# Kernel optimization log

Hardware: AMD Instinct MI355X
Metric: run time of the kernel (lower is better)

The kernel has to match this reference:

```python
import jax, jax.numpy as jnp
import numpy as np

H = 1024   # GRU hidden size
Z = 1024   # latent z dim
A = 4      # action dim
F = 30     # number of expert MLPs / max horizon
DIN = Z + H      # 2048, expert MLP input
DH = 512         # expert MLP hidden
EIN = H + 94     # evalMLP input (belief + pos/ori one-hot)
EH = 512
EOUT = 94


def setup_inputs() -> dict:
    key = jax.random.key(0)
    ks = jax.random.split(key, 20)
    s = 0.02
    inp = {
        "b_t": jax.random.normal(ks[0], (1, H), jnp.float32),
        "a_t": jax.random.normal(ks[1], (F, A), jnp.float32),
        "z_tp1_pos": jax.random.normal(ks[2], (F, Z), jnp.float32),
        "z_tp1_neg": jax.random.normal(ks[3], (F, Z), jnp.float32),
        "init_pos_ori": jax.random.uniform(ks[4], (1, 94), jnp.float32),
        # action GRU params (PyTorch layout: W_ih (3H, A), W_hh (3H, H))
        "gru_Wih": jax.random.normal(ks[5], (3 * H, A), jnp.float32) * s,
        "gru_Whh": jax.random.normal(ks[6], (3 * H, H), jnp.float32) * s,
        "gru_bih": jax.random.normal(ks[7], (3 * H,), jnp.float32) * s,
        "gru_bhh": jax.random.normal(ks[8], (3 * H,), jnp.float32) * s,
        # 30 stacked expert MLPs: Linear(DIN,DH)+ReLU+Linear(DH,1)
        "mlp_W1": jax.random.normal(ks[9], (F, DIN, DH), jnp.float32) * s,
        "mlp_b1": jax.random.normal(ks[10], (F, DH), jnp.float32) * s,
        "mlp_W2": jax.random.normal(ks[11], (F, DH, 1), jnp.float32) * s,
        "mlp_b2": jax.random.normal(ks[12], (F, 1), jnp.float32) * s,
        # evalMLP: Linear(EIN,EH)+ReLU+Linear(EH,EOUT)+sigmoid
        "eval_W1": jax.random.normal(ks[13], (EIN, EH), jnp.float32) * s,
        "eval_b1": jax.random.normal(ks[14], (EH,), jnp.float32) * s,
        "eval_W2": jax.random.normal(ks[15], (EH, EOUT), jnp.float32) * s,
        "eval_b2": jax.random.normal(ks[16], (EOUT,), jnp.float32) * s,
        "f": F,
    }
    return inp


def _gru(x, h0, Wih, Whh, bih, bhh):
    # x: (T, A), h0: (H,) -> outputs (T, H). PyTorch nn.GRU cell math.
    def step(h, xt):
        gi = Wih @ xt + bih          # (3H,)
        gh = Whh @ h + bhh           # (3H,)
        ir, iz, inn = jnp.split(gi, 3)
        hr, hz, hn = jnp.split(gh, 3)
        r = jax.nn.sigmoid(ir + hr)
        z = jax.nn.sigmoid(iz + hz)
        n = jnp.tanh(inn + r * hn)
        h_new = (1.0 - z) * n + z * h
        return h_new, h_new
    _, hs = jax.lax.scan(step, h0, x)
    return hs


def _experts(x, W1, b1, W2, b2, f):
    # x: (f, DIN); expert i applied to row i only (grouped batch-1 GEMMs).
    h = jax.nn.relu(jnp.einsum('fi,fih->fh', x, W1[:f]) + b1[:f])
    return jnp.einsum('fh,fho->fo', h, W2[:f]) + b2[:f]   # (f, 1) logits


def reference(b_t, a_t, z_tp1_pos, z_tp1_neg, init_pos_ori,
              gru_Wih, gru_Whh, gru_bih, gru_bhh,
              mlp_W1, mlp_b1, mlp_W2, mlp_b2,
              eval_W1, eval_b1, eval_W2, eval_b2, f):
    a_gru = _gru(a_t[:f], b_t[0], gru_Wih, gru_Whh, gru_bih, gru_bhh)  # (f, H)
    z_pos = jnp.concatenate([z_tp1_pos[:f], a_gru], axis=1)           # (f, Z+H)
    pred_positive = _experts(z_pos, mlp_W1, mlp_b1, mlp_W2, mlp_b2, f)
    z_neg = jnp.concatenate([z_tp1_neg[:f], a_gru], axis=1)
    pred_negative = _experts(z_neg, mlp_W1, mlp_b1, mlp_W2, mlp_b2, f)
    # eval branch uses b_t.detach()
    eval_in = jnp.concatenate([jax.lax.stop_gradient(b_t), init_pos_ori], axis=1)
    eh = jax.nn.relu(eval_in @ eval_W1 + eval_b1)
    pred_xytheta = jax.nn.sigmoid(eh @ eval_W2 + eval_b2)             # (1, 94)
    return pred_positive, pred_negative, pred_xytheta
```

## Files before the change

### kernel.cpp

```cpp
#include <hip/hip_runtime.h>
#include <math.h>

constexpr int kH    = 1024;
constexpr int kZ    = 1024;
constexpr int kA    = 4;
constexpr int kF    = 30;
constexpr int kDIN  = 2048;
constexpr int kDH   = 512;
constexpr int kEIN  = 1118;
constexpr int kEH   = 512;
constexpr int kEOUT = 94;

constexpr size_t GI_OFF   = 0;
constexpr size_t AGRU_OFF = GI_OFF + (size_t)kF*3*kH;
constexpr size_t HACC_OFF = AGRU_OFF + (size_t)kF*kH;
constexpr size_t EHA_OFF  = HACC_OFF + (size_t)kF*2*kDH;

__device__ __forceinline__ float sigmoidf_(float x) { return 1.0f / (1.0f + __expf(-x)); }

__device__ __forceinline__ float wave_reduce(float v) {
#pragma unroll
  for (int off = 32; off > 0; off >>= 1) v += __shfl_down(v, off, 64);
  return v;
}

__global__ __launch_bounds__(256) void gi_kernel(const float* __restrict__ Wih,
                                                 const float* __restrict__ bih,
                                                 const float* __restrict__ a_t,
                                                 float* __restrict__ gi,
                                                 const int* __restrict__ fptr) {
  int idx = blockIdx.x * 256 + threadIdx.x;
  if (idx >= kF * 3 * kH) return;
  int t = idx / (3 * kH);
  int r = idx - t * (3 * kH);
  if (t >= *fptr) return;
  float acc = bih[r];
#pragma unroll
  for (int k = 0; k < kA; k++) acc += Wih[r * kA + k] * a_t[t * kA + k];
  gi[idx] = acc;
}

__global__ __launch_bounds__(256) void gru_step(const float* __restrict__ Whh,
                                                const float* __restrict__ bhh,
                                                const float* __restrict__ gi,
                                                const float* __restrict__ b_t,
                                                float* __restrict__ agru,
                                                int t,
                                                const int* __restrict__ fptr) {
  if (t >= *fptr) return;
  const float* hprev = (t == 0) ? b_t : (agru + (size_t)(t - 1) * kH);
  int wave = threadIdx.x >> 6;
  int lane = threadIdx.x & 63;
  int j = blockIdx.x * 4 + wave;

  const float4* wr = (const float4*)(Whh + (size_t)j * kH);
  const float4* wz = (const float4*)(Whh + (size_t)(j + kH) * kH);
  const float4* wn = (const float4*)(Whh + (size_t)(j + 2 * kH) * kH);
  const float4* hv = (const float4*)hprev;

  float accr = 0.f, accz = 0.f, accn = 0.f;
#pragma unroll
  for (int k = lane; k < kH / 4; k += 64) {
    float4 hh = hv[k];
    float4 a = wr[k]; accr += a.x * hh.x + a.y * hh.y + a.z * hh.z + a.w * hh.w;
    float4 b = wz[k]; accz += b.x * hh.x + b.y * hh.y + b.z * hh.z + b.w * hh.w;
    float4 c = wn[k]; accn += c.x * hh.x + c.y * hh.y + c.z * hh.z + c.w * hh.w;
  }
  accr = wave_reduce(accr);
  accz = wave_reduce(accz);
  accn = wave_reduce(accn);

  if (lane == 0) {
    const float* git = gi + (size_t)t * 3 * kH;
    float gr = git[j] + accr + bhh[j];
    float gz = git[kH + j] + accz + bhh[kH + j];
    float hn = accn + bhh[2 * kH + j];
    float inn = git[2 * kH + j];
    float r = sigmoidf_(gr);
    float z = sigmoidf_(gz);
    float n = tanhf(inn + r * hn);
    agru[(size_t)t * kH + j] = (1.0f - z) * n + z * hprev[j];
  }
}

constexpr int EXP_SPLIT = 8;
constexpr int EVAL_SPLIT = 8;

__global__ __launch_bounds__(512) void stage1(const float* __restrict__ zpos,
                                              const float* __restrict__ zneg,
                                              const float* __restrict__ agru,
                                              const float* __restrict__ W1,
                                              const float* __restrict__ b_t,
                                              const float* __restrict__ ipo,
                                              const float* __restrict__ eW1,
                                              float* __restrict__ hacc,
                                              float* __restrict__ ehacc,
                                              const int* __restrict__ fptr) {
  int b = blockIdx.x;
  int tid = threadIdx.x;
  __shared__ float xs_p[256];
  __shared__ float xs_n[256];

  if (b < kF * EXP_SPLIT) {
    int i = b >> 3;
    int part = b & 7;
    if (i >= *fptr) return;
    int r0 = part * 256;
    if (tid < 256) {
      int r = r0 + tid;
      float xp, xn;
      if (r < kZ) { xp = zpos[(size_t)i * kZ + r]; xn = zneg[(size_t)i * kZ + r]; }
      else        { float v = agru[(size_t)i * kH + (r - kZ)]; xp = v; xn = v; }
      xs_p[tid] = xp;
      xs_n[tid] = xn;
    }
    __syncthreads();
    float ap = 0.f, an = 0.f;
    const float* w = W1 + ((size_t)i * kDIN + r0) * kDH + tid;
#pragma unroll 4
    for (int r = 0; r < 256; r++) {
      float wv = w[(size_t)r * kDH];
      ap += xs_p[r] * wv;
      an += xs_n[r] * wv;
    }
    atomicAdd(&hacc[((size_t)i * 2 + 0) * kDH + tid], ap);
    atomicAdd(&hacc[((size_t)i * 2 + 1) * kDH + tid], an);
  } else {
    int part = b - kF * EXP_SPLIT;
    int r0 = part * 140;
    int nrows = min(140, kEIN - r0);
    if (tid < nrows) {
      int r = r0 + tid;
      xs_p[tid < 256 ? tid : 0] = 0.f;
    }
    __shared__ float xs[140];
    if (tid < nrows) {
      int r = r0 + tid;
      xs[tid] = (r < kH) ? b_t[r] : ipo[r - kH];
    }
    __syncthreads();
    float acc = 0.f;
    const float* w = eW1 + (size_t)r0 * kEH + tid;
    for (int r = 0; r < nrows; r++) acc += xs[r] * w[(size_t)r * kEH];
    atomicAdd(&ehacc[tid], acc);
  }
}

__global__ __launch_bounds__(512) void stage2(const float* __restrict__ hacc,
                                              const float* __restrict__ ehacc,
                                              const float* __restrict__ b1,
                                              const float* __restrict__ W2,
                                              const float* __restrict__ b2,
                                              const float* __restrict__ eb1,
                                              const float* __restrict__ eW2,
                                              const float* __restrict__ eb2,
                                              float* __restrict__ out,
                                              const int* __restrict__ fptr) {
  int b = blockIdx.x;
  int tid = threadIdx.x;
  int f = *fptr;
  if (b < kF) {
    int i = b;
    if (i >= f) return;
    float bias = b1[(size_t)i * kDH + tid];
    float hp = fmaxf(hacc[((size_t)i * 2 + 0) * kDH + tid] + bias, 0.f);
    float hn = fmaxf(hacc[((size_t)i * 2 + 1) * kDH + tid] + bias, 0.f);
    float w = W2[(size_t)i * kDH + tid];
    float pp = hp * w, pn = hn * w;
    pp = wave_reduce(pp);
    pn = wave_reduce(pn);
    __shared__ float redp[8];
    __shared__ float redn[8];
    int wave = tid >> 6, lane = tid & 63;
    if (lane == 0) { redp[wave] = pp; redn[wave] = pn; }
    __syncthreads();
    if (tid == 0) {
      float sp = 0.f, sn = 0.f;
#pragma unroll
      for (int k = 0; k < 8; k++) { sp += redp[k]; sn += redn[k]; }
      out[i] = sp + b2[i];
      out[f + i] = sn + b2[i];
    }
  } else {
    if (tid < kEOUT) {
      float acc = eb2[tid];
      for (int h = 0; h < kEH; h++) {
        float eh = fmaxf(ehacc[h] + eb1[h], 0.f);
        acc += eh * eW2[(size_t)h * kEOUT + tid];
      }
      out[2 * f + tid] = sigmoidf_(acc);
    }
  }
}

extern "C" void kernel_launch(void* const* d_in, const int* in_sizes, int n_in,
                              void* d_out, int out_size, void* d_ws, size_t ws_size,
                              hipStream_t stream) {
  const float* b_t    = (const float*)d_in[0];
  const float* a_t    = (const float*)d_in[1];
  const float* zpos   = (const float*)d_in[2];
  const float* zneg   = (const float*)d_in[3];
  const float* ipo    = (const float*)d_in[4];
  const float* gWih   = (const float*)d_in[5];
  const float* gWhh   = (const float*)d_in[6];
  const float* gbih   = (const float*)d_in[7];
  const float* gbhh   = (const float*)d_in[8];
  const float* mW1    = (const float*)d_in[9];
  const float* mb1    = (const float*)d_in[10];
  const float* mW2    = (const float*)d_in[11];
  const float* mb2    = (const float*)d_in[12];
  const float* eW1    = (const float*)d_in[13];
  const float* eb1    = (const float*)d_in[14];
  const float* eW2    = (const float*)d_in[15];
  const float* eb2    = (const float*)d_in[16];
  const int*   fptr   = (const int*)d_in[17];

  float* ws   = (float*)d_ws;
  float* gi   = ws + GI_OFF;
  float* agru = ws + AGRU_OFF;
  float* hacc = ws + HACC_OFF;
  float* ehacc= ws + EHA_OFF;
  float* out  = (float*)d_out;

  hipMemsetAsync(hacc, 0, (size_t)(kF * 2 * kDH + kEH) * sizeof(float), stream);

  gi_kernel<<<(kF * 3 * kH + 255) / 256, 256, 0, stream>>>(gWih, gbih, a_t, gi, fptr);

  for (int t = 0; t < kF; t++) {
    gru_step<<<kH / 4, 256, 0, stream>>>(gWhh, gbhh, gi, b_t, agru, t, fptr);
  }

  stage1<<<kF * EXP_SPLIT + EVAL_SPLIT, 512, 0, stream>>>(zpos, zneg, agru, mW1, b_t,
                                                          ipo, eW1, hacc, ehacc, fptr);

  stage2<<<kF + 1, 512, 0, stream>>>(hacc, ehacc, mb1, mW2, mb2, eb1, eW2, eb2, out, fptr);
}
```

Baseline: 399.8 us.

## Replace per-step GRU launches with persistent kernel using grid barrier

The 30 separate gru_step launches and the gi_kernel are replaced by one persistent kernel of 64 blocks. Each block keeps its slice of the recurrent weights in registers, computes its input-gate projections up front into shared memory, and advances timesteps with a global atomic counter barrier. This is meant to remove per-timestep launch overhead and repeated weight reloads from memory. It depends on all 64 blocks being resident at once and adds the cost of a spin barrier on every step.

Result: slower. 445.2 us (+11.3%).

```diff
diff --git a/kernel.cpp b/kernel.cpp
--- a/kernel.cpp
+++ b/kernel.cpp
@@ -11,10 +11,14 @@
 constexpr int kEH   = 512;
 constexpr int kEOUT = 94;
 
-constexpr size_t GI_OFF   = 0;
-constexpr size_t AGRU_OFF = GI_OFF + (size_t)kF*3*kH;
-constexpr size_t HACC_OFF = AGRU_OFF + (size_t)kF*kH;
-constexpr size_t EHA_OFF  = HACC_OFF + (size_t)kF*2*kDH;
+constexpr int NB  = 64;
+constexpr int BT  = 1024;
+constexpr int JPB = 16;
+
+constexpr size_t AGRU_OFF = 0;
+constexpr size_t HACC_OFF = AGRU_OFF + (size_t)kF * kH;
+constexpr size_t EHA_OFF  = HACC_OFF + (size_t)kF * 2 * kDH;
+constexpr size_t BAR_OFF  = EHA_OFF + kEH;
 
 __device__ __forceinline__ float sigmoidf_(float x) { return 1.0f / (1.0f + __expf(-x)); }
 
@@ -24,66 +28,91 @@
   return v;
 }
 
-__global__ __launch_bounds__(256) void gi_kernel(const float* __restrict__ Wih,
-                                                 const float* __restrict__ bih,
-                                                 const float* __restrict__ a_t,
-                                                 float* __restrict__ gi,
-                                                 const int* __restrict__ fptr) {
-  int idx = blockIdx.x * 256 + threadIdx.x;
-  if (idx >= kF * 3 * kH) return;
-  int t = idx / (3 * kH);
-  int r = idx - t * (3 * kH);
-  if (t >= *fptr) return;
-  float acc = bih[r];
-#pragma unroll
-  for (int k = 0; k < kA; k++) acc += Wih[r * kA + k] * a_t[t * kA + k];
-  gi[idx] = acc;
-}
-
-__global__ __launch_bounds__(256) void gru_step(const float* __restrict__ Whh,
-                                                const float* __restrict__ bhh,
-                                                const float* __restrict__ gi,
-                                                const float* __restrict__ b_t,
-                                                float* __restrict__ agru,
-                                                int t,
-                                                const int* __restrict__ fptr) {
-  if (t >= *fptr) return;
-  const float* hprev = (t == 0) ? b_t : (agru + (size_t)(t - 1) * kH);
-  int wave = threadIdx.x >> 6;
-  int lane = threadIdx.x & 63;
-  int j = blockIdx.x * 4 + wave;
-
-  const float4* wr = (const float4*)(Whh + (size_t)j * kH);
-  const float4* wz = (const float4*)(Whh + (size_t)(j + kH) * kH);
-  const float4* wn = (const float4*)(Whh + (size_t)(j + 2 * kH) * kH);
-  const float4* hv = (const float4*)hprev;
-
-  float accr = 0.f, accz = 0.f, accn = 0.f;
-#pragma unroll
-  for (int k = lane; k < kH / 4; k += 64) {
-    float4 hh = hv[k];
-    float4 a = wr[k]; accr += a.x * hh.x + a.y * hh.y + a.z * hh.z + a.w * hh.w;
-    float4 b = wz[k]; accz += b.x * hh.x + b.y * hh.y + b.z * hh.z + b.w * hh.w;
-    float4 c = wn[k]; accn += c.x * hh.x + c.y * hh.y + c.z * hh.z + c.w * hh.w;
-  }
-  accr = wave_reduce(accr);
-  accz = wave_reduce(accz);
-  accn = wave_reduce(accn);
-
-  if (lane == 0) {
-    const float* git = gi + (size_t)t * 3 * kH;
-    float gr = git[j] + accr + bhh[j];
-    float gz = git[kH + j] + accz + bhh[kH + j];
-    float hn = accn + bhh[2 * kH + j];
-    float inn = git[2 * kH + j];
-    float r = sigmoidf_(gr);
-    float z = sigmoidf_(gz);
-    float n = tanhf(inn + r * hn);
-    agru[(size_t)t * kH + j] = (1.0f - z) * n + z * hprev[j];
-  }
-}
-
-constexpr int EXP_SPLIT = 8;
+__global__ __launch_bounds__(BT) void gru_persist(const float* __restrict__ Whh,
+                                                  const float* __restrict__ bhh,
+                                                  const float* __restrict__ Wih,
+                                                  const float* __restrict__ bih,
+                                                  const float* __restrict__ a_t,
+                                                  const float* __restrict__ b_t,
+                                                  float* __restrict__ agru,
+                                                  unsigned* __restrict__ bar,
+                                                  const int* __restrict__ fptr) {
+  const int tid  = threadIdx.x;
+  const int wave = tid >> 6;
+  const int lane = tid & 63;
+  const int j    = blockIdx.x * JPB + wave;
+  const int f    = *fptr;
+
+  const float4* W4 = (const float4*)Whh;
+  float4 wr[4], wz[4], wn[4];
+#pragma unroll
+  for (int i = 0; i < 4; i++) {
+    wr[i] = W4[(size_t)j * 256 + i * 64 + lane];
+    wz[i] = W4[(size_t)(j + kH) * 256 + i * 64 + lane];
+    wn[i] = W4[(size_t)(j + 2 * kH) * 256 + i * 64 + lane];
+  }
+  const float bhr = bhh[j];
+  const float bhz = bhh[j + kH];
+  const float bhn = bhh[j + 2 * kH];
+
+  __shared__ float gis[kF][JPB][3];
+  __shared__ __align__(16) float hs[kH];
+  for (int idx = tid; idx < kF * JPB * 3; idx += BT) {
+    int t = idx / (JPB * 3);
+    int rem = idx - t * (JPB * 3);
+    int w = rem / 3, g = rem - w * 3;
+    int r = blockIdx.x * JPB + w + g * kH;
+    float acc = bih[r];
+    const float* wih = Wih + (size_t)r * kA;
+    const float* at  = a_t + (size_t)t * kA;
+#pragma unroll
+    for (int k = 0; k < kA; k++) acc += wih[k] * at[k];
+    gis[t][w][g] = acc;
+  }
+  __syncthreads();
+
+  const float4* hs4 = (const float4*)hs;
+
+  for (int t = 0; t < f; t++) {
+    const float* hsrc = (t == 0) ? b_t : (agru + (size_t)(t - 1) * kH);
+    hs[tid] = __hip_atomic_load(hsrc + tid, __ATOMIC_RELAXED, __HIP_MEMORY_SCOPE_AGENT);
+    __syncthreads();
+
+    float accr = 0.f, accz = 0.f, accn = 0.f;
+#pragma unroll
+    for (int i = 0; i < 4; i++) {
+      float4 h4 = hs4[i * 64 + lane];
+      accr += wr[i].x * h4.x + wr[i].y * h4.y + wr[i].z * h4.z + wr[i].w * h4.w;
+      accz += wz[i].x * h4.x + wz[i].y * h4.y + wz[i].z * h4.z + wz[i].w * h4.w;
+      accn += wn[i].x * h4.x + wn[i].y * h4.y + wn[i].z * h4.z + wn[i].w * h4.w;
+    }
+    accr = wave_reduce(accr);
+    accz = wave_reduce(accz);
+    accn = wave_reduce(accn);
+
+    if (lane == 0) {
+      float rg = sigmoidf_(gis[t][wave][0] + accr + bhr);
+      float zg = sigmoidf_(gis[t][wave][1] + accz + bhz);
+      float ng = tanhf(gis[t][wave][2] + rg * (accn + bhn));
+      float hnew = (1.0f - zg) * ng + zg * hs[j];
+      __hip_atomic_store(agru + (size_t)t * kH + j, hnew, __ATOMIC_RELAXED,
+                         __HIP_MEMORY_SCOPE_AGENT);
+    }
+
+    __syncthreads();
+    if (tid == 0) {
+      __threadfence();
+      __hip_atomic_fetch_add(bar, 1u, __ATOMIC_ACQ_REL, __HIP_MEMORY_SCOPE_AGENT);
+      const unsigned target = (unsigned)NB * (unsigned)(t + 1);
+      while (__hip_atomic_load(bar, __ATOMIC_ACQUIRE, __HIP_MEMORY_SCOPE_AGENT) < target) {
+        __builtin_amdgcn_s_sleep(1);
+      }
+    }
+    __syncthreads();
+  }
+}
+
+constexpr int EXP_SPLIT  = 8;
 constexpr int EVAL_SPLIT = 8;
 
 __global__ __launch_bounds__(512) void stage1(const float* __restrict__ zpos,
@@ -98,10 +127,10 @@
                                               const int* __restrict__ fptr) {
   int b = blockIdx.x;
   int tid = threadIdx.x;
-  __shared__ float xs_p[256];
-  __shared__ float xs_n[256];
 
   if (b < kF * EXP_SPLIT) {
+    __shared__ float xs_p[256];
+    __shared__ float xs_n[256];
     int i = b >> 3;
     int part = b & 7;
     if (i >= *fptr) return;
@@ -126,14 +155,10 @@
     atomicAdd(&hacc[((size_t)i * 2 + 0) * kDH + tid], ap);
     atomicAdd(&hacc[((size_t)i * 2 + 1) * kDH + tid], an);
   } else {
+    __shared__ float xs[140];
     int part = b - kF * EXP_SPLIT;
     int r0 = part * 140;
     int nrows = min(140, kEIN - r0);
-    if (tid < nrows) {
-      int r = r0 + tid;
-      xs_p[tid < 256 ? tid : 0] = 0.f;
-    }
-    __shared__ float xs[140];
     if (tid < nrows) {
       int r = r0 + tid;
       xs[tid] = (r < kH) ? b_t[r] : ipo[r - kH];
@@ -166,9 +191,8 @@
     float hp = fmaxf(hacc[((size_t)i * 2 + 0) * kDH + tid] + bias, 0.f);
     float hn = fmaxf(hacc[((size_t)i * 2 + 1) * kDH + tid] + bias, 0.f);
     float w = W2[(size_t)i * kDH + tid];
-    float pp = hp * w, pn = hn * w;
-    pp = wave_reduce(pp);
-    pn = wave_reduce(pn);
+    float pp = wave_reduce(hp * w);
+    float pn = wave_reduce(hn * w);
     __shared__ float redp[8];
     __shared__ float redn[8];
     int wave = tid >> 6, lane = tid & 63;
@@ -196,39 +220,35 @@
 extern "C" void kernel_launch(void* const* d_in, const int* in_sizes, int n_in,
                               void* d_out, int out_size, void* d_ws, size_t ws_size,
                               hipStream_t stream) {
-  const float* b_t    = (const float*)d_in[0];
-  const float* a_t    = (const float*)d_in[1];
-  const float* zpos   = (const float*)d_in[2];
-  const float* zneg   = (const float*)d_in[3];
-  const float* ipo    = (const float*)d_in[4];
-  const float* gWih   = (const float*)d_in[5];
-  const float* gWhh   = (const float*)d_in[6];
-  const float* gbih   = (const float*)d_in[7];
-  const float* gbhh   = (const float*)d_in[8];
-  const float* mW1    = (const float*)d_in[9];
-  const float* mb1    = (const float*)d_in[10];
-  const float* mW2    = (const float*)d_in[11];
-  const float* mb2    = (const float*)d_in[12];
-  const float* eW1    = (const float*)d_in[13];
-  const float* eb1    = (const float*)d_in[14];
-  const float* eW2    = (const float*)d_in[15];
-  const float* eb2    = (const float*)d_in[16];
-  const int*   fptr   = (const int*)d_in[17];
-
-  float* ws   = (float*)d_ws;
-  float* gi   = ws + GI_OFF;
-  float* agru = ws + AGRU_OFF;
-  float* hacc = ws + HACC_OFF;
-  float* ehacc= ws + EHA_OFF;
-  float* out  = (float*)d_out;
-
-  hipMemsetAsync(hacc, 0, (size_t)(kF * 2 * kDH + kEH) * sizeof(float), stream);
-
-  gi_kernel<<<(kF * 3 * kH + 255) / 256, 256, 0, stream>>>(gWih, gbih, a_t, gi, fptr);
-
-  for (int t = 0; t < kF; t++) {
-    gru_step<<<kH / 4, 256, 0, stream>>>(gWhh, gbhh, gi, b_t, agru, t, fptr);
-  }
+  const float* b_t  = (const float*)d_in[0];
+  const float* a_t  = (const float*)d_in[1];
+  const float* zpos = (const float*)d_in[2];
+  const float* zneg = (const float*)d_in[3];
+  const float* ipo  = (const float*)d_in[4];
+  const float* gWih = (const float*)d_in[5];
+  const float* gWhh = (const float*)d_in[6];
+  const float* gbih = (const float*)d_in[7];
+  const float* gbhh = (const float*)d_in[8];
+  const float* mW1  = (const float*)d_in[9];
+  const float* mb1  = (const float*)d_in[10];
+  const float* mW2  = (const float*)d_in[11];
+  const float* mb2  = (const float*)d_in[12];
+  const float* eW1  = (const float*)d_in[13];
+  const float* eb1  = (const float*)d_in[14];
+  const float* eW2  = (const float*)d_in[15];
+  const float* eb2  = (const float*)d_in[16];
+  const int*   fptr = (const int*)d_in[17];
+
+  float* ws    = (float*)d_ws;
+  float* agru  = ws + AGRU_OFF;
+  float* hacc  = ws + HACC_OFF;
+  float* ehacc = ws + EHA_OFF;
+  unsigned* bar = (unsigned*)(ws + BAR_OFF);
+  float* out   = (float*)d_out;
+
+  hipMemsetAsync(hacc, 0, ((size_t)kF * 2 * kDH + kEH + 1) * sizeof(float), stream);
+
+  gru_persist<<<NB, BT, 0, stream>>>(gWhh, gbhh, gWih, gbih, a_t, b_t, agru, bar, fptr);
 
   stage1<<<kF * EXP_SPLIT + EVAL_SPLIT, 512, 0, stream>>>(zpos, zneg, agru, mW1, b_t,
                                                           ipo, eW1, hacc, ehacc, fptr);
```
